# Kernel optimization log

Hardware: AMD Instinct MI355X
Metric: run time of the kernel (lower is better)

## Reference

```python
import jax, jax.numpy as jnp
import numpy as np
from jax import lax

NB_ITER = 100
TOL = 1e-6
DN = ('NCHW', 'OIHW', 'NCHW')
PAD = ((1, 1), (1, 1))


def _P(x, kernel):
    # x: [B,H,W] -> [B,3,H,W], conv2d with kernel [3,1,3,3], padding=1
    return lax.conv_general_dilated(x[:, None], kernel, (1, 1), PAD, dimension_numbers=DN)


def _PT(x, kernel):
    # x: [B,3,H,W] -> [B,H,W]; conv_transpose2d(padding=1) == conv2d with
    # spatially-flipped kernel and in/out channels swapped.
    kt = jnp.flip(kernel, (2, 3)).transpose(1, 0, 2, 3)  # [1,3,3,3]
    return lax.conv_general_dilated(x, kt, (1, 1), PAD, dimension_numbers=DN)[:, 0]


def _cg(A, b):
    # Conjugate gradient; original: while i <= 100 and crit >= tol (101 iters max).
    x = b
    r = b - A(x)
    p = r
    crit = jnp.sum(r * r)

    def body(carry, _):
        x, r, p, crit = carry
        active = crit >= TOL
        Ap = A(p)
        denom = jnp.sum(p * Ap)
        alpha = crit / jnp.where(active, denom, 1.0)
        x_n = x + alpha * p
        r_n = r - alpha * Ap
        crit_n = jnp.sum(r_n * r_n)
        beta = crit_n / jnp.where(active, crit, 1.0)
        p_n = r_n + beta * p
        x = jnp.where(active, x_n, x)
        r = jnp.where(active, r_n, r)
        p = jnp.where(active, p_n, p)
        crit = jnp.where(active, crit_n, crit)
        return (x, r, p, crit), None

    (x, _, _, _), _ = lax.scan(body, (x, r, p, crit), None, length=NB_ITER + 1)
    return x


def setup_inputs() -> dict:
    key = jax.random.key(0)
    ks = jax.random.split(key, 6)
    B, C, H, W = 4, 3, 256, 256
    return {
        'mask': jax.random.uniform(ks[0], (B, C, H, W), dtype=jnp.float32),
        'y': jax.random.uniform(ks[1], (B, H, W), dtype=jnp.float32),
        'z': jax.random.normal(ks[2], (B, C, H, W), dtype=jnp.float32),
        'beta': jax.random.normal(ks[3], (B, C, H, W), dtype=jnp.float32),
        'rho': jnp.float32(0.1),
        'kernel': jax.random.uniform(ks[4], (3, 1, 3, 3), dtype=jnp.float32),
    }


def reference(mask, y, z, beta, rho, kernel):
    def A(x):
        # rho*x + adjoint(mask, PT(P(direct(mask, x))))
        d = jnp.sum(mask * x, axis=1)                 # [B,H,W]
        return rho * x + mask * _PT(_P(d, kernel), kernel)[:, None]

    b = mask * _PT(_P(y, kernel), kernel)[:, None] + rho * (z - beta)
    return _cg(A, b)
```

## Files before the change

### kernel.cpp

```cpp
#include <hip/hip_runtime.h>

#define TOL 1e-6f
#define NITER 101
#define H 256
#define W 256
#define HW 65536
#define NBLK 256
#define TPB 256

typedef unsigned long long ull;

#define STRIP_F 768
#define STRIPBUF (NBLK * STRIP_F)
#define WS_CTRL (2 * STRIPBUF)
#define CTRL_F 8192

#define LD_AG(p)    __hip_atomic_load((p), __ATOMIC_RELAXED, __HIP_MEMORY_SCOPE_AGENT)
#define ST_AG(p,v)  __hip_atomic_store((p), (v), __ATOMIC_RELAXED, __HIP_MEMORY_SCOPE_AGENT)

__device__ __forceinline__ unsigned opq0u() {
    unsigned z; asm volatile("s_mov_b32 %0, 0" : "=s"(z)); return z;
}
__device__ __forceinline__ ull opq0ull() {
    return ((ull)opq0u() << 32) | (ull)opq0u();
}
__device__ __forceinline__ float opq0f() { return __uint_as_float(opq0u()); }

__device__ __forceinline__ float2 frb2(float va, float vb, unsigned rnd, float* ctrl,
                                       unsigned my_xcc, unsigned xn, unsigned ng) {
    __shared__ float redA_[4], redB_[4], out_[2];
    asm volatile("s_waitcnt vmcnt(0)" ::: "memory");
    #pragma unroll
    for (int off = 32; off; off >>= 1) {
        va += __shfl_down(va, off, 64);
        vb += __shfl_down(vb, off, 64);
    }
    const int lane = threadIdx.x & 63, wid = threadIdx.x >> 6;
    if (lane == 0) { redA_[wid] = va; redB_[wid] = vb; }
    __syncthreads();
    if (threadIdx.x == 0) {
        const float pa = redA_[0] + redA_[1] + redA_[2] + redA_[3];
        const float pb = redB_[0] + redB_[1] + redB_[2] + redB_[3];
        const unsigned sub = (blockIdx.x >> 3) & 3u;
        float* gvalA = ctrl;
        float* gvalB = ctrl + 256;
        float* lvalA = ctrl + 512  + my_xcc * 256;
        float* lvalB = ctrl + 2560 + my_xcc * 256;
        unsigned* cu = (unsigned*)(ctrl + 4608);
        ull* bcastA = (ull*)(cu + 320);
        ull* bcastB = (ull*)(cu + 448);
        ull* lbcA   = (ull*)(cu + 576);
        ull* lbcB   = (ull*)(cu + 1088);
        __hip_atomic_fetch_add(lvalA + rnd, pa, __ATOMIC_RELAXED, __HIP_MEMORY_SCOPE_WORKGROUP);
        __hip_atomic_fetch_add(lvalB + rnd, pb, __ATOMIC_RELAXED, __HIP_MEMORY_SCOPE_WORKGROUP);
        asm volatile("s_waitcnt vmcnt(0)" ::: "memory");
        unsigned a = __hip_atomic_fetch_add(cu + my_xcc * 16, 1u,
                         __ATOMIC_RELAXED, __HIP_MEMORY_SCOPE_WORKGROUP);
        ull pkA, pkB;
        if (a == rnd * xn - 1u) {
            float la = __hip_atomic_fetch_add(lvalA + rnd, opq0f(),
                           __ATOMIC_RELAXED, __HIP_MEMORY_SCOPE_WORKGROUP);
            float lb = __hip_atomic_fetch_add(lvalB + rnd, opq0f(),
                           __ATOMIC_RELAXED, __HIP_MEMORY_SCOPE_WORKGROUP);
            __hip_atomic_fetch_add(gvalA + rnd, la, __ATOMIC_RELAXED, __HIP_MEMORY_SCOPE_AGENT);
            __hip_atomic_fetch_add(gvalB + rnd, lb, __ATOMIC_RELAXED, __HIP_MEMORY_SCOPE_AGENT);
            asm volatile("s_waitcnt vmcnt(0)" ::: "memory");
            unsigned g = __hip_atomic_fetch_add(cu + 128, 1u,
                             __ATOMIC_RELAXED, __HIP_MEMORY_SCOPE_AGENT);
            if (g == rnd * ng - 1u) {
                float ta = __hip_atomic_fetch_add(gvalA + rnd, opq0f(),
                               __ATOMIC_RELAXED, __HIP_MEMORY_SCOPE_AGENT);
                float tb = __hip_atomic_fetch_add(gvalB + rnd, opq0f(),
                               __ATOMIC_RELAXED, __HIP_MEMORY_SCOPE_AGENT);
                pkA = ((ull)rnd << 32) | (ull)__float_as_uint(ta);
                pkB = ((ull)rnd << 32) | (ull)__float_as_uint(tb);
                #pragma unroll
                for (int xx = 0; xx < 8; ++xx)
                    __hip_atomic_store(bcastB + xx * 8, pkB,
                                       __ATOMIC_RELAXED, __HIP_MEMORY_SCOPE_AGENT);
                #pragma unroll
                for (int xx = 0; xx < 8; ++xx)
                    __hip_atomic_store(bcastA + xx * 8, pkA,
                                       __ATOMIC_RELAXED, __HIP_MEMORY_SCOPE_AGENT);
            } else {
                for (;;) {
                    pkA = __hip_atomic_fetch_add(bcastA + my_xcc * 8, opq0ull(),
                              __ATOMIC_RELAXED, __HIP_MEMORY_SCOPE_AGENT);
                    if ((unsigned)(pkA >> 32) >= rnd) break;
                }
                for (;;) {
                    pkB = __hip_atomic_fetch_add(bcastB + my_xcc * 8, opq0ull(),
                              __ATOMIC_RELAXED, __HIP_MEMORY_SCOPE_AGENT);
                    if ((unsigned)(pkB >> 32) >= rnd) break;
                }
            }
            #pragma unroll
            for (int s = 0; s < 4; ++s)
                __hip_atomic_store(lbcB + (my_xcc * 4 + s) * 8, pkB,
                                   __ATOMIC_RELAXED, __HIP_MEMORY_SCOPE_WORKGROUP);
            #pragma unroll
            for (int s = 0; s < 4; ++s)
                __hip_atomic_store(lbcA + (my_xcc * 4 + s) * 8, pkA,
                                   __ATOMIC_RELAXED, __HIP_MEMORY_SCOPE_WORKGROUP);
        } else {
            ull* mylA = lbcA + (my_xcc * 4 + sub) * 8;
            ull* mylB = lbcB + (my_xcc * 4 + sub) * 8;
            for (;;) {
                pkA = __hip_atomic_fetch_add(mylA, opq0ull(),
                          __ATOMIC_RELAXED, __HIP_MEMORY_SCOPE_WORKGROUP);
                if ((unsigned)(pkA >> 32) >= rnd) break;
                __builtin_amdgcn_s_sleep(2);
            }
            for (;;) {
                pkB = __hip_atomic_fetch_add(mylB, opq0ull(),
                          __ATOMIC_RELAXED, __HIP_MEMORY_SCOPE_WORKGROUP);
                if ((unsigned)(pkB >> 32) >= rnd) break;
                __builtin_amdgcn_s_sleep(1);
            }
        }
        out_[0] = __uint_as_float((unsigned)(pkA & 0xffffffffull));
        out_[1] = __uint_as_float((unsigned)(pkB & 0xffffffffull));
    }
    __syncthreads();
    return make_float2(out_[0], out_[1]);
}

__device__ __forceinline__ void ring_pos(int t, int& eh, int& ew) {
    if (t < 72)       { eh = t / 36;                 ew = t - (t / 36) * 36; }
    else if (t < 144) { const int u = t - 72;  eh = 34 + u / 36; ew = u - (u / 36) * 36; }
    else              { const int u = t - 144; eh = 2 + (u >> 2);
                        const int c2 = u & 3;  ew = (c2 < 2) ? c2 : c2 + 32; }
}

__device__ __forceinline__ float4 conv_k2(const float* dext, int row, int wb,
                                          int h0, int w0,
                                          const float* K2sh,
                                          const float* Ctop, const float* Cbot,
                                          const float* CLf, const float* CLt, const float* CLb,
                                          const float* CRf, const float* CRt, const float* CRb)
{
    float q[4] = {0.f, 0.f, 0.f, 0.f};
    float w2s[8], cL[5], cR[5];
    const float* base = dext + row * 36 + wb;
    #pragma unroll
    for (int A = 0; A < 5; ++A) {
        const float4 lo = *(const float4*)(base + A * 36);
        const float4 hi = *(const float4*)(base + A * 36 + 4);
        const float w8[8] = {lo.x, lo.y, lo.z, lo.w, hi.x, hi.y, hi.z, hi.w};
        #pragma unroll
        for (int cc = 0; cc < 4; ++cc) {
            float s = q[cc];
            #pragma unroll
            for (int Bq = 0; Bq < 5; ++Bq)
                s += K2sh[A * 5 + Bq] * w8[cc + Bq];
            q[cc] = s;
        }
        if (A == 2) {
            #pragma unroll
            for (int u = 0; u < 8; ++u) w2s[u] = w8[u];
        }
        cL[A] = w8[2]; cR[A] = w8[5];
    }
    const int gh = h0 + row, gwb = w0 + wb;
    if (gh == 0) {
        #pragma unroll
        for (int cc = 0; cc < 4; ++cc)
            #pragma unroll
            for (int Bq = 0; Bq < 5; ++Bq)
                q[cc] -= Ctop[Bq] * w2s[cc + Bq];
    }
    if (gh == 255) {
        #pragma unroll
        for (int cc = 0; cc < 4; ++cc)
            #pragma unroll
            for (int Bq = 0; Bq < 5; ++Bq)
                q[cc] -= Cbot[Bq] * w2s[cc + Bq];
    }
    if (gwb == 0) {
        const float* C = (gh == 0) ? CLt : ((gh == 255) ? CLb : CLf);
        #pragma unroll
        for (int A = 0; A < 5; ++A) q[0] -= C[A] * cL[A];
    }
    if (gwb == 252) {
        const float* C = (gh == 0) ? CRt : ((gh == 255) ? CRb : CRf);
        #pragma unroll
        for (int A = 0; A < 5; ++A) q[3] -= C[A] * cR[A];
    }
    return make_float4(q[0], q[1], q[2], q[3]);
}

extern "C" __global__ void __launch_bounds__(TPB)
cg_persistent(const float* __restrict__ mask, const float* __restrict__ y,
              const float* __restrict__ z, const float* __restrict__ bet,
              const float* __restrict__ rho_p, const float* __restrict__ kern,
              float* __restrict__ x_out, float* __restrict__ ws)
{
    __shared__ float ksh[27];
    __shared__ __align__(16) float dext[36 * 36];
    __shared__ float m_ring[3][272];
    __shared__ float r_ring[3][272];
    __shared__ float q_ring[3][272];
    __shared__ float sstage[STRIP_F];
    __shared__ int   ringsrc[272];
    __shared__ float K2sh[25];
    __shared__ float Ctop[5], Cbot[5];
    __shared__ float CLf[5], CLt[5], CLb[5], CRf[5], CRt[5], CRb[5];

    float* strip = ws;
    float* ctrl  = ws + WS_CTRL;

    const int tid = threadIdx.x;
    const int T  = blockIdx.x;
    const int bi = T >> 6;
    const int h0 = ((T >> 3) & 7) << 5;
    const int w0 = (T & 7) << 5;
    const int row = tid >> 3;
    const int wb  = (tid & 7) << 2;
    const int roffb = (h0 + row) * W + (w0 + wb);

    unsigned xcc_raw;
    asm volatile("s_getreg_b32 %0, hwreg(HW_REG_XCC_ID)" : "=s"(xcc_raw));
    const unsigned my_xcc = xcc_raw & 7u;

    unsigned xn = 0, ng = 0;
    unsigned* cu = (unsigned*)(ctrl + 4608);
    if (tid == 0) {
        __hip_atomic_fetch_add(cu + 160 + 16 * my_xcc, 1u,
                               __ATOMIC_RELAXED, __HIP_MEMORY_SCOPE_AGENT);
        __hip_atomic_fetch_add(cu + 144, 1u,
                               __ATOMIC_RELAXED, __HIP_MEMORY_SCOPE_AGENT);
    }

    if (tid < 27) ksh[tid] = kern[tid];
    const float rho = rho_p[0];

    float m_[3][4], x_[3][4], r_[3][4], p_[3][4], q_[3][4], w_[3][4];
    #pragma unroll
    for (int c = 0; c < 3; ++c) {
        const float4 mv = *(const float4*)(mask + (bi * 3 + c) * HW + roffb);
        m_[c][0] = mv.x; m_[c][1] = mv.y; m_[c][2] = mv.z; m_[c][3] = mv.w;
    }

    for (int t = tid; t < 272; t += TPB) {
        int eh, ew; ring_pos(t, eh, ew);
        const int gh = h0 + eh - 2, gw = w0 + ew - 2;
        const bool valid = (unsigned)gh < (unsigned)H && (unsigned)gw < (unsigned)W;
        int src = -1;
        if (valid) {
            const int tr = gh >> 5, tc = gw >> 5;
            const int Tn = (bi << 6) | (tr << 3) | tc;
            const int lh = gh & 31, lw = gw & 31;
            int idx;
            if (tr != (h0 >> 5)) idx = (lh >= 30) ? 64 + (lh - 30) * 32 + lw : lh * 32 + lw;
            else                 idx = (lw >= 30) ? 192 + lh * 2 + (lw - 30) : 128 + lh * 2 + lw;
            src = Tn * STRIP_F + idx;
        }
        ringsrc[t] = src;
        #pragma unroll
        for (int c = 0; c < 3; ++c) {
            m_ring[c][t] = valid ? mask[(bi * 3 + c) * HW + gh * W + gw] : 0.f;
            r_ring[c][t] = 0.f;
            q_ring[c][t] = 0.f;
        }
    }

    for (int e = tid; e < 1296; e += TPB) {
        const int eh = e / 36, ew = e - eh * 36;
        const int gh = h0 + eh - 2, gw = w0 + ew - 2;
        dext[e] = ((unsigned)gh < (unsigned)H && (unsigned)gw < (unsigned)W)
                      ? y[bi * HW + gh * W + gw] : 0.f;
    }
    __syncthreads();

    if (tid < 25) {
        const int A = tid / 5, Bq = tid % 5;
        float s = 0.f;
        for (int o = 0; o < 3; ++o)
            for (int i = (A > 2 ? A - 2 : 0); i <= (A < 2 ? A : 2); ++i)
                for (int j = (Bq > 2 ? Bq - 2 : 0); j <= (Bq < 2 ? Bq : 2); ++j)
                    s += ksh[o * 9 + (A - i) * 3 + (Bq - j)] * ksh[o * 9 + (2 - i) * 3 + (2 - j)];
        K2sh[tid] = s;
    } else if (tid < 35) {
        const int Bq = (tid - 25) % 5;
        const int krow = (tid < 30) ? 6 : 0;
        float s = 0.f;
        for (int o = 0; o < 3; ++o)
            for (int j = (Bq > 2 ? Bq - 2 : 0); j <= (Bq < 2 ? Bq : 2); ++j)
                s += ksh[o * 9 + krow + (Bq - j)] * ksh[o * 9 + krow + (2 - j)];
        if (tid < 30) Ctop[Bq] = s; else Cbot[Bq] = s;
    } else if (tid < 65) {
        const int u = tid - 35;
        const int side = u / 15;
        const int v = (u % 15) / 5;
        const int A = u % 5;
        const int kcol = side ? 0 : 2;
        int ilo = (A > 2 ? A - 2 : 0), ihi = (A < 2 ? A : 2);
        if (v == 1 && ilo < 1) ilo = 1;
        if (v == 2 && ihi > 1) ihi = 1;
        float s = 0.f;
        for (int o = 0; o < 3; ++o)
            for (int i = ilo; i <= ihi; ++i)
                s += ksh[o * 9 + (A - i) * 3 + kcol] * ksh[o * 9 + (2 - i) * 3 + kcol];
        float* dst = side ? (v == 0 ? CRf : v == 1 ? CRt : CRb)
                          : (v == 0 ? CLf : v == 1 ? CLt : CLb);
        dst[A] = s;
    }
    __syncthreads();

#define STAGE_BORDER(SRC)                                                          \
    _Pragma("unroll")                                                              \
    for (int c = 0; c < 3; ++c) {                                                  \
        if (row < 2) {                                                             \
            _Pragma("unroll")                                                      \
            for (int cc = 0; cc < 4; ++cc)                                         \
                sstage[c * 256 + row * 32 + wb + cc] = SRC[c][cc];                 \
        }                                                                          \
        if (row >= 30) {                                                           \
            _Pragma("unroll")                                                      \
            for (int cc = 0; cc < 4; ++cc)                                         \
                sstage[c * 256 + 64 + (row - 30) * 32 + wb + cc] = SRC[c][cc];     \
        }                                                                          \
        if (wb == 0)  { sstage[c * 256 + 128 + row * 2]     = SRC[c][0];           \
                        sstage[c * 256 + 128 + row * 2 + 1] = SRC[c][1]; }         \
        if (wb == 28) { sstage[c * 256 + 192 + row * 2]     = SRC[c][2];           \
                        sstage[c * 256 + 192 + row * 2 + 1] = SRC[c][3]; }         \
    }

    {
        const float4 qv = conv_k2(dext, row, wb, h0, w0, K2sh, Ctop, Cbot,
                                  CLf, CLt, CLb, CRf, CRt, CRb);
        const float qa[4] = {qv.x, qv.y, qv.z, qv.w};
        #pragma unroll
        for (int c = 0; c < 3; ++c) {
            const int gi = (bi * 3 + c) * HW + roffb;
            const float4 zv = *(const float4*)(z + gi);
            const float4 bv = *(const float4*)(bet + gi);
            const float zz[4] = {zv.x, zv.y, zv.z, zv.w};
            const float bb[4] = {bv.x, bv.y, bv.z, bv.w};
            #pragma unroll
            for (int cc = 0; cc < 4; ++cc)
                x_[c][cc] = m_[c][cc] * qa[cc] + rho * (zz[cc] - bb[cc]);
        }
    }
    STAGE_BORDER(x_)
    __syncthreads();
    for (int t = tid; t < STRIP_F; t += TPB)
        ST_AG(strip + T * STRIP_F + t, sstage[t]);

    if (tid == 0) {
        while (__hip_atomic_fetch_add(cu + 144, opq0u(), __ATOMIC_RELAXED,
                                      __HIP_MEMORY_SCOPE_AGENT) < (unsigned)NBLK)
            __builtin_amdgcn_s_sleep(32);
        ng = 0;
        #pragma unroll
        for (int i = 0; i < 8; ++i) {
            unsigned c = __hip_atomic_fetch_add(cu + 160 + 16 * i, opq0u(),
                             __ATOMIC_RELAXED, __HIP_MEMORY_SCOPE_AGENT);
            ng += (c > 0u);
        }
        xn = __hip_atomic_fetch_add(cu + 160 + 16 * my_xcc, opq0u(),
                 __ATOMIC_RELAXED, __HIP_MEMORY_SCOPE_AGENT);
    }
    unsigned rnd = 1;
    frb2(0.f, 0.f, rnd++, ctrl, my_xcc, xn, ng);

    {
        float* dp = dext + (row + 2) * 36 + 2 + wb;
        #pragma unroll
        for (int cc = 0; cc < 4; ++cc)
            dp[cc] = m_[0][cc] * x_[0][cc] + m_[1][cc] * x_[1][cc] + m_[2][cc] * x_[2][cc];
    }
    for (int t = tid; t < 272; t += TPB) {
        int eh, ew; ring_pos(t, eh, ew);
        const int src = ringsrc[t];
        float s = 0.f;
        if (src >= 0) {
            #pragma unroll
            for (int c = 0; c < 3; ++c)
                s += m_ring[c][t] * LD_AG(strip + src + c * 256);
        }
        dext[eh * 36 + ew] = s;
    }
    __syncthreads();
    float gsum0 = 0.f;
    {
        const float4 qv = conv_k2(dext, row, wb, h0, w0, K2sh, Ctop, Cbot,
                                  CLf, CLt, CLb, CRf, CRt, CRb);
        const float qa[4] = {qv.x, qv.y, qv.z, qv.w};
        #pragma unroll
        for (int c = 0; c < 3; ++c)
            #pragma unroll
            for (int cc = 0; cc < 4; ++cc) {
                const float b = x_[c][cc];
                const float rv = b - (rho * b + m_[c][cc] * qa[cc]);
                r_[c][cc] = rv; p_[c][cc] = rv;
                gsum0 += rv * rv;
            }
    }
    STAGE_BORDER(r_)
    __syncthreads();
    for (int t = tid; t < STRIP_F; t += TPB)
        ST_AG(strip + STRIPBUF + T * STRIP_F + t, sstage[t]);

    float gamma = frb2(gsum0, 0.f, rnd++, ctrl, my_xcc, xn, ng).x;

    for (int t = tid; t < 272; t += TPB) {
        const int src = ringsrc[t];
        if (src >= 0) {
            #pragma unroll
            for (int c = 0; c < 3; ++c)
                r_ring[c][t] = LD_AG(strip + STRIPBUF + src + c * 256);
        }
    }

    {
        float* dp = dext + (row + 2) * 36 + 2 + wb;
        #pragma unroll
        for (int cc = 0; cc < 4; ++cc)
            dp[cc] = m_[0][cc] * r_[0][cc] + m_[1][cc] * r_[1][cc] + m_[2][cc] * r_[2][cc];
    }
    for (int t = tid; t < 272; t += TPB) {
        int eh, ew; ring_pos(t, eh, ew);
        float s = 0.f;
        #pragma unroll
        for (int c = 0; c < 3; ++c) s += m_ring[c][t] * r_ring[c][t];
        dext[eh * 36 + ew] = s;
    }
    __syncthreads();
    float dsum0 = 0.f;
    {
        const float4 qv = conv_k2(dext, row, wb, h0, w0, K2sh, Ctop, Cbot,
                                  CLf, CLt, CLb, CRf, CRt, CRb);
        const float qa[4] = {qv.x, qv.y, qv.z, qv.w};
        #pragma unroll
        for (int c = 0; c < 3; ++c)
            #pragma unroll
            for (int cc = 0; cc < 4; ++cc) {
                const float wv = rho * r_[c][cc] + m_[c][cc] * qa[cc];
                q_[c][cc] = wv;
                dsum0 += r_[c][cc] * wv;
            }
    }
    STAGE_BORDER(q_)
    __syncthreads();
    for (int t = tid; t < STRIP_F; t += TPB)
        ST_AG(strip + T * STRIP_F + t, sstage[t]);

    const float delta0 = frb2(dsum0, 0.f, rnd++, ctrl, my_xcc, xn, ng).x;

    for (int t = tid; t < 272; t += TPB) {
        const int src = ringsrc[t];
        if (src >= 0) {
            #pragma unroll
            for (int c = 0; c < 3; ++c)
                q_ring[c][t] = LD_AG(strip + src + c * 256);
        }
    }
    float alpha = (gamma >= TOL) ? (gamma / delta0) : 0.f;

    for (int j = 0; j < NITER; ++j) {
        const bool active = (gamma >= TOL);

        if (active) {
            #pragma unroll
            for (int c = 0; c < 3; ++c)
                #pragma unroll
                for (int cc = 0; cc < 4; ++cc) {
                    x_[c][cc] += alpha * p_[c][cc];
                    r_[c][cc] -= alpha * q_[c][cc];
                }
            for (int t = tid; t < 272; t += TPB) {
                #pragma unroll
                for (int c = 0; c < 3; ++c)
                    r_ring[c][t] -= alpha * q_ring[c][t];
            }
        }

        {
            float* dp = dext + (row + 2) * 36 + 2 + wb;
            #pragma unroll
            for (int cc = 0; cc < 4; ++cc)
                dp[cc] = m_[0][cc] * r_[0][cc] + m_[1][cc] * r_[1][cc] + m_[2][cc] * r_[2][cc];
        }
        for (int t = tid; t < 272; t += TPB) {
            int eh, ew; ring_pos(t, eh, ew);
            float s = 0.f;
            #pragma unroll
            for (int c = 0; c < 3; ++c) s += m_ring[c][t] * r_ring[c][t];
            dext[eh * 36 + ew] = s;
        }
        __syncthreads();
        float gsum = 0.f, dsum = 0.f;
        {
            const float4 qv = conv_k2(dext, row, wb, h0, w0, K2sh, Ctop, Cbot,
                                      CLf, CLt, CLb, CRf, CRt, CRb);
            const float qa[4] = {qv.x, qv.y, qv.z, qv.w};
            #pragma unroll
            for (int c = 0; c < 3; ++c)
                #pragma unroll
                for (int cc = 0; cc < 4; ++cc) {
                    const float rv = r_[c][cc];
                    const float wv = rho * rv + m_[c][cc] * qa[cc];
                    w_[c][cc] = wv;
                    gsum += rv * rv;
                    dsum += rv * wv;
                }
        }
        STAGE_BORDER(w_)
        __syncthreads();
        float* gb = strip + ((j + 1) & 1) * STRIPBUF;
        for (int t = tid; t < STRIP_F; t += TPB)
            ST_AG(gb + T * STRIP_F + t, sstage[t]);

        const float2 gd = frb2(gsum, dsum, rnd++, ctrl, my_xcc, xn, ng);

        if (active) {
            const float gp = gd.x, dp = gd.y;
            const float beta = gp / gamma;
            const float alphan = gp / (dp - beta * gp / alpha);
            #pragma unroll
            for (int c = 0; c < 3; ++c)
                #pragma unroll
                for (int cc = 0; cc < 4; ++cc) {
                    p_[c][cc] = r_[c][cc] + beta * p_[c][cc];
                    q_[c][cc] = w_[c][cc] + beta * q_[c][cc];
                }
            for (int t = tid; t < 272; t += TPB) {
                const int src = ringsrc[t];
                if (src >= 0) {
                    #pragma unroll
                    for (int c = 0; c < 3; ++c) {
                        const float wn = LD_AG(gb + src + c * 256);
                        q_ring[c][t] = wn + beta * q_ring[c][t];
                    }
                }
            }
            gamma = gp;
            alpha = alphan;
        }
    }

    #pragma unroll
    for (int c = 0; c < 3; ++c)
        *(float4*)(x_out + (bi * 3 + c) * HW + roffb) =
            make_float4(x_[c][0], x_[c][1], x_[c][2], x_[c][3]);
}

extern "C" void kernel_launch(void* const* d_in, const int* in_sizes, int n_in,
                              void* d_out, int out_size, void* d_ws, size_t ws_size,
                              hipStream_t stream)
{
    const float* mask = (const float*)d_in[0];
    const float* y    = (const float*)d_in[1];
    const float* z    = (const float*)d_in[2];
    const float* bet  = (const float*)d_in[3];
    const float* rho  = (const float*)d_in[4];
    const float* kern = (const float*)d_in[5];
    float* x  = (float*)d_out;
    float* ws = (float*)d_ws;

    hipMemsetAsync(ws + WS_CTRL, 0, CTRL_F * sizeof(float), stream);

    void* args[] = { (void*)&mask, (void*)&y, (void*)&z, (void*)&bet,
                     (void*)&rho, (void*)&kern, (void*)&x, (void*)&ws };
    hipLaunchCooperativeKernel((void*)cg_persistent, dim3(NBLK), dim3(TPB),
                               args, 0, stream);
}
```

Measured before the change: 1.070 ms.

## Split global reduction into arrive/wait and overlap halo fetch with it

```diff
diff --git a/kernel.cpp b/kernel.cpp
--- a/kernel.cpp
+++ b/kernel.cpp
@@ -13,7 +13,7 @@
 #define STRIP_F 768
 #define STRIPBUF (NBLK * STRIP_F)
 #define WS_CTRL (2 * STRIPBUF)
-#define CTRL_F 8192
+#define CTRL_F 16384
 
 #define LD_AG(p)    __hip_atomic_load((p), __ATOMIC_RELAXED, __HIP_MEMORY_SCOPE_AGENT)
 #define ST_AG(p,v)  __hip_atomic_store((p), (v), __ATOMIC_RELAXED, __HIP_MEMORY_SCOPE_AGENT)
@@ -26,9 +26,12 @@
 }
 __device__ __forceinline__ float opq0f() { return __uint_as_float(opq0u()); }
 
-__device__ __forceinline__ float2 frb2(float va, float vb, unsigned rnd, float* ctrl,
-                                       unsigned my_xcc, unsigned xn, unsigned ng) {
-    __shared__ float redA_[4], redB_[4], out_[2];
+struct FrbTok { unsigned role; ull pkA, pkB; };
+
+__device__ __forceinline__ FrbTok frb2_arrive(float va, float vb, unsigned rnd,
+                                              float* ctrl, unsigned my_xcc,
+                                              unsigned xn, unsigned ng) {
+    __shared__ float redA_[4], redB_[4];
     asm volatile("s_waitcnt vmcnt(0)" ::: "memory");
     #pragma unroll
     for (int off = 32; off; off >>= 1) {
@@ -38,10 +41,10 @@
     const int lane = threadIdx.x & 63, wid = threadIdx.x >> 6;
     if (lane == 0) { redA_[wid] = va; redB_[wid] = vb; }
     __syncthreads();
+    FrbTok tk; tk.role = 0u; tk.pkA = 0ull; tk.pkB = 0ull;
     if (threadIdx.x == 0) {
         const float pa = redA_[0] + redA_[1] + redA_[2] + redA_[3];
         const float pb = redB_[0] + redB_[1] + redB_[2] + redB_[3];
-        const unsigned sub = (blockIdx.x >> 3) & 3u;
         float* gvalA = ctrl;
         float* gvalB = ctrl + 256;
         float* lvalA = ctrl + 512  + my_xcc * 256;
@@ -56,8 +59,8 @@
         asm volatile("s_waitcnt vmcnt(0)" ::: "memory");
         unsigned a = __hip_atomic_fetch_add(cu + my_xcc * 16, 1u,
                          __ATOMIC_RELAXED, __HIP_MEMORY_SCOPE_WORKGROUP);
-        ull pkA, pkB;
         if (a == rnd * xn - 1u) {
+            tk.role = 1u;
             float la = __hip_atomic_fetch_add(lvalA + rnd, opq0f(),
                            __ATOMIC_RELAXED, __HIP_MEMORY_SCOPE_WORKGROUP);
             float lb = __hip_atomic_fetch_add(lvalB + rnd, opq0f(),
@@ -68,31 +71,57 @@
             unsigned g = __hip_atomic_fetch_add(cu + 128, 1u,
                              __ATOMIC_RELAXED, __HIP_MEMORY_SCOPE_AGENT);
             if (g == rnd * ng - 1u) {
+                tk.role = 2u;
                 float ta = __hip_atomic_fetch_add(gvalA + rnd, opq0f(),
                                __ATOMIC_RELAXED, __HIP_MEMORY_SCOPE_AGENT);
                 float tb = __hip_atomic_fetch_add(gvalB + rnd, opq0f(),
                                __ATOMIC_RELAXED, __HIP_MEMORY_SCOPE_AGENT);
-                pkA = ((ull)rnd << 32) | (ull)__float_as_uint(ta);
-                pkB = ((ull)rnd << 32) | (ull)__float_as_uint(tb);
+                tk.pkA = ((ull)rnd << 32) | (ull)__float_as_uint(ta);
+                tk.pkB = ((ull)rnd << 32) | (ull)__float_as_uint(tb);
                 #pragma unroll
                 for (int xx = 0; xx < 8; ++xx)
-                    __hip_atomic_store(bcastB + xx * 8, pkB,
+                    __hip_atomic_store(bcastB + xx * 8, tk.pkB,
                                        __ATOMIC_RELAXED, __HIP_MEMORY_SCOPE_AGENT);
                 #pragma unroll
                 for (int xx = 0; xx < 8; ++xx)
-                    __hip_atomic_store(bcastA + xx * 8, pkA,
+                    __hip_atomic_store(bcastA + xx * 8, tk.pkA,
                                        __ATOMIC_RELAXED, __HIP_MEMORY_SCOPE_AGENT);
-            } else {
-                for (;;) {
-                    pkA = __hip_atomic_fetch_add(bcastA + my_xcc * 8, opq0ull(),
-                              __ATOMIC_RELAXED, __HIP_MEMORY_SCOPE_AGENT);
-                    if ((unsigned)(pkA >> 32) >= rnd) break;
-                }
-                for (;;) {
-                    pkB = __hip_atomic_fetch_add(bcastB + my_xcc * 8, opq0ull(),
-                              __ATOMIC_RELAXED, __HIP_MEMORY_SCOPE_AGENT);
-                    if ((unsigned)(pkB >> 32) >= rnd) break;
-                }
+                #pragma unroll
+                for (int s = 0; s < 4; ++s)
+                    __hip_atomic_store(lbcB + (my_xcc * 4 + s) * 8, tk.pkB,
+                                       __ATOMIC_RELAXED, __HIP_MEMORY_SCOPE_WORKGROUP);
+                #pragma unroll
+                for (int s = 0; s < 4; ++s)
+                    __hip_atomic_store(lbcA + (my_xcc * 4 + s) * 8, tk.pkA,
+                                       __ATOMIC_RELAXED, __HIP_MEMORY_SCOPE_WORKGROUP);
+            }
+        }
+    }
+    return tk;
+}
+
+__device__ __forceinline__ float2 frb2_wait(FrbTok tk, unsigned rnd, float* ctrl,
+                                            unsigned my_xcc) {
+    __shared__ float outw_[2];
+    if (threadIdx.x == 0) {
+        unsigned* cu = (unsigned*)(ctrl + 4608);
+        ull* bcastA = (ull*)(cu + 320);
+        ull* bcastB = (ull*)(cu + 448);
+        ull* lbcA   = (ull*)(cu + 576);
+        ull* lbcB   = (ull*)(cu + 1088);
+        const unsigned sub = (blockIdx.x >> 3) & 3u;
+        ull pkA, pkB;
+        if (tk.role == 2u) { pkA = tk.pkA; pkB = tk.pkB; }
+        else if (tk.role == 1u) {
+            for (;;) {
+                pkA = __hip_atomic_fetch_add(bcastA + my_xcc * 8, opq0ull(),
+                          __ATOMIC_RELAXED, __HIP_MEMORY_SCOPE_AGENT);
+                if ((unsigned)(pkA >> 32) >= rnd) break;
+            }
+            for (;;) {
+                pkB = __hip_atomic_fetch_add(bcastB + my_xcc * 8, opq0ull(),
+                          __ATOMIC_RELAXED, __HIP_MEMORY_SCOPE_AGENT);
+                if ((unsigned)(pkB >> 32) >= rnd) break;
             }
             #pragma unroll
             for (int s = 0; s < 4; ++s)
@@ -118,11 +147,11 @@
                 __builtin_amdgcn_s_sleep(1);
             }
         }
-        out_[0] = __uint_as_float((unsigned)(pkA & 0xffffffffull));
-        out_[1] = __uint_as_float((unsigned)(pkB & 0xffffffffull));
-    }
-    __syncthreads();
-    return make_float2(out_[0], out_[1]);
+        outw_[0] = __uint_as_float((unsigned)(pkA & 0xffffffffull));
+        outw_[1] = __uint_as_float((unsigned)(pkB & 0xffffffffull));
+    }
+    __syncthreads();
+    return make_float2(outw_[0], outw_[1]);
 }
 
 __device__ __forceinline__ void ring_pos(int t, int& eh, int& ew) {
@@ -200,8 +229,11 @@
     __shared__ float m_ring[3][272];
     __shared__ float r_ring[3][272];
     __shared__ float q_ring[3][272];
+    __shared__ float u_ring[3][272];
     __shared__ float sstage[STRIP_F];
     __shared__ int   ringsrc[272];
+    __shared__ int   nbl[8];
+    __shared__ int   nn_sh;
     __shared__ float K2sh[25];
     __shared__ float Ctop[5], Cbot[5];
     __shared__ float CLf[5], CLt[5], CLb[5], CRf[5], CRt[5], CRb[5];
@@ -224,11 +256,22 @@
 
     unsigned xn = 0, ng = 0;
     unsigned* cu = (unsigned*)(ctrl + 4608);
+    ull* flg = (ull*)(cu + 2048);
     if (tid == 0) {
         __hip_atomic_fetch_add(cu + 160 + 16 * my_xcc, 1u,
                                __ATOMIC_RELAXED, __HIP_MEMORY_SCOPE_AGENT);
         __hip_atomic_fetch_add(cu + 144, 1u,
                                __ATOMIC_RELAXED, __HIP_MEMORY_SCOPE_AGENT);
+        int n = 0;
+        const int tr0 = (T >> 3) & 7, tc0 = T & 7;
+        for (int dr = -1; dr <= 1; ++dr)
+            for (int dc = -1; dc <= 1; ++dc) {
+                if (dr == 0 && dc == 0) continue;
+                const int tr = tr0 + dr, tc = tc0 + dc;
+                if ((unsigned)tr < 8u && (unsigned)tc < 8u)
+                    nbl[n++] = (bi << 6) | (tr << 3) | tc;
+            }
+        nn_sh = n;
     }
 
     if (tid < 27) ksh[tid] = kern[tid];
@@ -261,6 +304,7 @@
             m_ring[c][t] = valid ? mask[(bi * 3 + c) * HW + gh * W + gw] : 0.f;
             r_ring[c][t] = 0.f;
             q_ring[c][t] = 0.f;
+            u_ring[c][t] = 0.f;
         }
     }
 
@@ -362,7 +406,8 @@
                  __ATOMIC_RELAXED, __HIP_MEMORY_SCOPE_AGENT);
     }
     unsigned rnd = 1;
-    frb2(0.f, 0.f, rnd++, ctrl, my_xcc, xn, ng);
+    frb2_wait(frb2_arrive(0.f, 0.f, rnd, ctrl, my_xcc, xn, ng), rnd, ctrl, my_xcc);
+    rnd++;
 
     {
         float* dp = dext + (row + 2) * 36 + 2 + wb;
@@ -402,7 +447,9 @@
     for (int t = tid; t < STRIP_F; t += TPB)
         ST_AG(strip + STRIPBUF + T * STRIP_F + t, sstage[t]);
 
-    float gamma = frb2(gsum0, 0.f, rnd++, ctrl, my_xcc, xn, ng).x;
+    float gamma = frb2_wait(frb2_arrive(gsum0, 0.f, rnd, ctrl, my_xcc, xn, ng),
+                            rnd, ctrl, my_xcc).x;
+    rnd++;
 
     for (int t = tid; t < 272; t += TPB) {
         const int src = ringsrc[t];
@@ -446,7 +493,9 @@
     for (int t = tid; t < STRIP_F; t += TPB)
         ST_AG(strip + T * STRIP_F + t, sstage[t]);
 
-    const float delta0 = frb2(dsum0, 0.f, rnd++, ctrl, my_xcc, xn, ng).x;
+    const float delta0 = frb2_wait(frb2_arrive(dsum0, 0.f, rnd, ctrl, my_xcc, xn, ng),
+                                   rnd, ctrl, my_xcc).x;
+    rnd++;
 
     for (int t = tid; t < 272; t += TPB) {
         const int src = ringsrc[t];
@@ -508,11 +557,38 @@
         }
         STAGE_BORDER(w_)
         __syncthreads();
-        float* gb = strip + ((j + 1) & 1) * STRIPBUF;
+        const unsigned par = (unsigned)((j + 1) & 1);
+        float* gb = strip + par * STRIPBUF;
         for (int t = tid; t < STRIP_F; t += TPB)
             ST_AG(gb + T * STRIP_F + t, sstage[t]);
 
-        const float2 gd = frb2(gsum, dsum, rnd++, ctrl, my_xcc, xn, ng);
+        FrbTok tk = frb2_arrive(gsum, dsum, rnd, ctrl, my_xcc, xn, ng);
+
+        if (tid == 0)
+            __hip_atomic_store(flg + (par * 256 + T) * 8,
+                               ((ull)rnd << 32) | 1ull,
+                               __ATOMIC_RELAXED, __HIP_MEMORY_SCOPE_AGENT);
+        if (tid < nn_sh) {
+            ull* f = flg + (par * 256 + nbl[tid]) * 8;
+            for (;;) {
+                ull pk = __hip_atomic_fetch_add(f, opq0ull(),
+                             __ATOMIC_RELAXED, __HIP_MEMORY_SCOPE_AGENT);
+                if ((unsigned)(pk >> 32) >= rnd) break;
+                __builtin_amdgcn_s_sleep(1);
+            }
+        }
+        __syncthreads();
+        for (int t = tid; t < 272; t += TPB) {
+            const int src = ringsrc[t];
+            if (src >= 0) {
+                #pragma unroll
+                for (int c = 0; c < 3; ++c)
+                    u_ring[c][t] = LD_AG(gb + src + c * 256);
+            }
+        }
+
+        const float2 gd = frb2_wait(tk, rnd, ctrl, my_xcc);
+        rnd++;
 
         if (active) {
             const float gp = gd.x, dp = gd.y;
@@ -526,13 +602,10 @@
                     q_[c][cc] = w_[c][cc] + beta * q_[c][cc];
                 }
             for (int t = tid; t < 272; t += TPB) {
-                const int src = ringsrc[t];
-                if (src >= 0) {
+                if (ringsrc[t] >= 0) {
                     #pragma unroll
-                    for (int c = 0; c < 3; ++c) {
-                        const float wn = LD_AG(gb + src + c * 256);
-                        q_ring[c][t] = wn + beta * q_ring[c][t];
-                    }
+                    for (int c = 0; c < 3; ++c)
+                        q_ring[c][t] = u_ring[c][t] + beta * q_ring[c][t];
                 }
             }
             gamma = gp;
```

New measurement: 1.060 ms. No clear change (-1.0%).
